# Optimization experiments

Measured on AMD Instinct MI355X. Metric: run time of the kernel, lower is better.

The kernel has to match this reference:

```python
import jax, jax.numpy as jnp
import numpy as np

B, S, D, H = 2, 2048, 1024, 16
DH = D // H
DFF = 4 * D
EPS = 1e-5


def layernorm(x, g, b):
    mu = jnp.mean(x, axis=-1, keepdims=True)
    var = jnp.mean(jnp.square(x - mu), axis=-1, keepdims=True)
    return (x - mu) * jax.lax.rsqrt(var + EPS) * g + b


def setup_inputs() -> dict:
    key = jax.random.key(0)
    ks = jax.random.split(key, 12)
    s = 0.02
    return {
        "x": jax.random.normal(ks[0], (B, S, D), dtype=jnp.float32),
        "ln1_g": jnp.ones((D,), jnp.float32),
        "ln1_b": jnp.zeros((D,), jnp.float32),
        "Wq": jax.random.normal(ks[1], (D, D), jnp.float32) * s,
        "bq": jnp.zeros((D,), jnp.float32),
        "Wk": jax.random.normal(ks[2], (D, D), jnp.float32) * s,
        "bk": jnp.zeros((D,), jnp.float32),
        "Wv": jax.random.normal(ks[3], (D, D), jnp.float32) * s,
        "bv": jnp.zeros((D,), jnp.float32),
        "Wo": jax.random.normal(ks[4], (D, D), jnp.float32) * s,
        "bo": jnp.zeros((D,), jnp.float32),
        "ln2_g": jnp.ones((D,), jnp.float32),
        "ln2_b": jnp.zeros((D,), jnp.float32),
        "W1": jax.random.normal(ks[5], (D, DFF), jnp.float32) * s,
        "b1": jnp.zeros((DFF,), jnp.float32),
        "W2": jax.random.normal(ks[6], (DFF, D), jnp.float32) * s,
        "b2": jnp.zeros((D,), jnp.float32),
    }


def block(x, ln1_g, ln1_b, Wq, bq, Wk, bk, Wv, bv, Wo, bo, ln2_g, ln2_b, W1, b1, W2, b2):
    h = layernorm(x, ln1_g, ln1_b)
    # projections -> [B, H, S, DH]
    q = (h @ Wq + bq).reshape(B, S, H, DH).transpose(0, 2, 1, 3)
    k = (h @ Wk + bk).reshape(B, S, H, DH).transpose(0, 2, 1, 3)
    v = (h @ Wv + bv).reshape(B, S, H, DH).transpose(0, 2, 1, 3)
    scores = jnp.einsum('bhqd,bhkd->bhqk', q, k) / jnp.sqrt(jnp.float32(DH))
    causal = jnp.tril(jnp.ones((S, S), dtype=bool))  # True = keep
    scores = jnp.where(causal, scores, -jnp.inf)
    attn = jax.nn.softmax(scores, axis=-1)
    out = jnp.einsum('bhqk,bhkd->bhqd', attn, v)
    out = out.transpose(0, 2, 1, 3).reshape(B, S, D)
    x = x + out @ Wo + bo
    h2 = layernorm(x, ln2_g, ln2_b)
    ff = jax.nn.gelu(h2 @ W1 + b1, approximate=False) @ W2 + b2
    return x + ff


def reference(x, ln1_g, ln1_b, Wq, bq, Wk, bk, Wv, bv, Wo, bo, ln2_g, ln2_b, W1, b1, W2, b2):
    return block(x, ln1_g, ln1_b, Wq, bq, Wk, bk, Wv, bv, Wo, bo, ln2_g, ln2_b, W1, b1, W2, b2)
```

## Files before the change

kernel.cpp:

```cpp
#include <hip/hip_runtime.h>
#include <cstdint>
#include <cstddef>


#define DEV static __device__ __forceinline__

typedef unsigned short u16;
typedef __bf16 bf16x8 __attribute__((ext_vector_type(8)));
typedef u16    u16x8  __attribute__((ext_vector_type(8)));
typedef u16    u16x4  __attribute__((ext_vector_type(4)));
typedef float  f32x4  __attribute__((ext_vector_type(4)));

#define AEXP2(x) __builtin_amdgcn_exp2f(x)

DEV u16 f2bfh(float f) {
  return __builtin_bit_cast(u16, (__bf16)f);
}

DEV void gl16(const void* g, void* l) {
  __builtin_amdgcn_global_load_lds(
      (const __attribute__((address_space(1))) unsigned*)g,
      (__attribute__((address_space(3))) unsigned*)l, 16, 0, 0);
}

__global__ __launch_bounds__(256)
void tconv(const float* __restrict__ in, u16* __restrict__ out, int R, int C)
{
  __shared__ float tile[32][33];
  const int tx = threadIdx.x & 31, ty = threadIdx.x >> 5;
  const int r0 = blockIdx.y * 32, c0 = blockIdx.x * 32;
#pragma unroll
  for (int i = 0; i < 4; ++i)
    tile[ty + 8*i][tx] = in[(size_t)(r0 + ty + 8*i) * C + c0 + tx];
  __syncthreads();
#pragma unroll
  for (int i = 0; i < 4; ++i)
    out[(size_t)(c0 + ty + 8*i) * R + r0 + tx] = f2bfh(tile[tx][ty + 8*i]);
}

__global__ __launch_bounds__(256)
void tconv4(const float* __restrict__ w0, const float* __restrict__ w1,
            const float* __restrict__ w2, const float* __restrict__ w3,
            u16* __restrict__ q0, u16* __restrict__ q1,
            u16* __restrict__ q2, u16* __restrict__ q3)
{
  __shared__ float tile[32][33];
  const int z = blockIdx.z;
  const float* in = z == 0 ? w0 : z == 1 ? w1 : z == 2 ? w2 : w3;
  u16* out       = z == 0 ? q0 : z == 1 ? q1 : z == 2 ? q2 : q3;
  const int tx = threadIdx.x & 31, ty = threadIdx.x >> 5;
  const int r0 = blockIdx.y * 32, c0 = blockIdx.x * 32;
#pragma unroll
  for (int i = 0; i < 4; ++i)
    tile[ty + 8*i][tx] = in[(size_t)(r0 + ty + 8*i) * 1024 + c0 + tx];
  __syncthreads();
#pragma unroll
  for (int i = 0; i < 4; ++i)
    out[(size_t)(c0 + ty + 8*i) * 1024 + r0 + tx] = f2bfh(tile[tx][ty + 8*i]);
}

__global__ __launch_bounds__(256)
void ln_fwd(const float* __restrict__ x, const float* __restrict__ g,
            const float* __restrict__ b, u16* __restrict__ out)
{
  const int row = blockIdx.x, t = threadIdx.x;
  const float4 v = ((const float4*)(x + (size_t)row * 1024))[t];
  float s1 = v.x + v.y + v.z + v.w;
  float s2 = v.x*v.x + v.y*v.y + v.z*v.z + v.w*v.w;
#pragma unroll
  for (int d = 1; d < 64; d <<= 1) {
    s1 += __shfl_xor(s1, d, 64);
    s2 += __shfl_xor(s2, d, 64);
  }
  __shared__ float sh[8];
  const int w = t >> 6;
  if ((t & 63) == 0) { sh[w] = s1; sh[w + 4] = s2; }
  __syncthreads();
  s1 = sh[0] + sh[1] + sh[2] + sh[3];
  s2 = sh[4] + sh[5] + sh[6] + sh[7];
  const float mu  = s1 * (1.0f / 1024.0f);
  const float var = s2 * (1.0f / 1024.0f) - mu * mu;
  const float rs  = rsqrtf(var + 1e-5f);
  const float4 gv = ((const float4*)g)[t];
  const float4 bv = ((const float4*)b)[t];
  u16x4 o;
  o[0] = f2bfh((v.x - mu) * rs * gv.x + bv.x);
  o[1] = f2bfh((v.y - mu) * rs * gv.y + bv.y);
  o[2] = f2bfh((v.z - mu) * rs * gv.z + bv.z);
  o[3] = f2bfh((v.w - mu) * rs * gv.w + bv.w);
  *(u16x4*)(out + (size_t)row * 1024 + t * 4) = o;
}

#define EPI_QKV  0
#define EPI_RES  1
#define EPI_GELU 2

#define QSCALE 0.180421f

template<int EPI>
__global__ __launch_bounds__(512, 2)
void gemm256(const u16* __restrict__ A, const u16* __restrict__ Bt,
             const float* __restrict__ b0, const float* __restrict__ b1,
             const float* __restrict__ b2,
             u16* __restrict__ o0, u16* __restrict__ o1, u16* __restrict__ o2,
             int N, int K)
{
  __shared__ u16 As[3][8192];
  __shared__ u16 Bs[3][8192];
  const int t = threadIdx.x, lane = t & 63, w = t >> 6;
  const int wr = w >> 2, wc = w & 3;
  const int d = blockIdx.x + gridDim.x * blockIdx.y;
  const int rr = d >> 3;
  const int m0 = ((d & 7) * 2 + (rr & 1)) * 256;
  const int n0 = (rr >> 1) * 256;
  const int li = lane & 15, lg = lane >> 4;

  const int srow = t >> 2;
  const int skc  = (t & 3) ^ ((t >> 3) & 3);
  const u16* Ag = A  + (size_t)(m0 + srow) * K + skc * 8;
  const u16* Bg = Bt + (size_t)(n0 + srow) * K + skc * 8;

  auto STG_A = [&](int k0, int b) {
#pragma unroll
    for (int p = 0; p < 2; ++p)
      gl16(Ag + k0 + (size_t)(p * 128) * K, &As[b][t * 8 + p * 4096]);
  };
  auto STG_B = [&](int k0, int b) {
#pragma unroll
    for (int p = 0; p < 2; ++p)
      gl16(Bg + k0 + (size_t)(p * 128) * K, &Bs[b][t * 8 + p * 4096]);
  };

  auto ldsoff = [](int R, int kc) {
    return (R >> 1) * 128 + (R & 1) * 64 + ((kc ^ ((R >> 1) & 3)) << 4);
  };

  f32x4 acc[8][4] = {};
  const int NT = K >> 5;

  STG_A(0, 0);  STG_B(0, 0);
  STG_A(32, 1); STG_B(32, 1);

  int cur = 0, nxt = 2;
  for (int kt = 0; kt < NT; ++kt) {
    if (kt + 1 < NT)
      asm volatile("s_waitcnt vmcnt(4)" ::: "memory");
    else
      asm volatile("s_waitcnt vmcnt(0)" ::: "memory");
    __builtin_amdgcn_s_barrier();
    __builtin_amdgcn_sched_barrier(0);

    const int k2 = (kt + 2) * 32;
    bf16x8 bfr[4], afA[4];
#pragma unroll
    for (int i = 0; i < 4; ++i)
      bfr[i] = *(const bf16x8*)((const char*)Bs[cur] +
                                ldsoff(wc * 64 + i * 16 + li, lg));
#pragma unroll
    for (int i = 0; i < 4; ++i)
      afA[i] = *(const bf16x8*)((const char*)As[cur] +
                                ldsoff(wr * 128 + i * 16 + li, lg));
    if (kt + 2 < NT) STG_A(k2, nxt);
    __builtin_amdgcn_s_setprio(1);
#pragma unroll
    for (int mi = 0; mi < 4; ++mi)
#pragma unroll
      for (int ni = 0; ni < 4; ++ni)
        acc[mi][ni] = __builtin_amdgcn_mfma_f32_16x16x32_bf16(
            afA[mi], bfr[ni], acc[mi][ni], 0, 0, 0);
    __builtin_amdgcn_s_setprio(0);

    bf16x8 afB[4];
#pragma unroll
    for (int i = 0; i < 4; ++i)
      afB[i] = *(const bf16x8*)((const char*)As[cur] +
                                ldsoff(wr * 128 + (4 + i) * 16 + li, lg));
    if (kt + 2 < NT) STG_B(k2, nxt);
    __builtin_amdgcn_s_setprio(1);
#pragma unroll
    for (int mi = 0; mi < 4; ++mi)
#pragma unroll
      for (int ni = 0; ni < 4; ++ni)
        acc[4 + mi][ni] = __builtin_amdgcn_mfma_f32_16x16x32_bf16(
            afB[mi], bfr[ni], acc[4 + mi][ni], 0, 0, 0);
    __builtin_amdgcn_s_setprio(0);

    cur = (cur + 1 == 3) ? 0 : cur + 1;
    nxt = (nxt + 1 == 3) ? 0 : nxt + 1;
  }

  const int crow = wr * 128 + lg * 4;
  const int ccol = wc * 64 + li;

  if (EPI == EPI_QKV) {
    const int which = n0 >> 10;
    const float* bias = which == 0 ? b0 : which == 1 ? b1 : b2;
    const int nn0 = n0 & 1023;
    if (which == 2) {
#pragma unroll
      for (int mi = 0; mi < 8; ++mi)
#pragma unroll
        for (int ni = 0; ni < 4; ++ni) {
          const int gm0 = m0 + crow + mi * 16;
          const int b_ = gm0 >> 11, s_ = gm0 & 2047;
          const int gc = nn0 + ccol + ni * 16;
          const int h_ = gc >> 6, d_ = gc & 63;
          u16x4 pk;
#pragma unroll
          for (int r = 0; r < 4; ++r) pk[r] = f2bfh(acc[mi][ni][r] + bias[gc]);
          *(u16x4*)(o2 + ((size_t)(b_ * 16 + h_) * 64 + d_) * 2048 + s_) = pk;
        }
    } else {
      u16* outp = which == 0 ? o0 : o1;
      const float sc = which == 0 ? QSCALE : 1.0f;
#pragma unroll
      for (int mi = 0; mi < 8; ++mi)
#pragma unroll
        for (int ni = 0; ni < 4; ++ni)
#pragma unroll
          for (int r = 0; r < 4; ++r) {
            const int gm = m0 + crow + mi * 16 + r;
            const int gc = nn0 + ccol + ni * 16;
            const float v = (acc[mi][ni][r] + bias[gc]) * sc;
            const int b_ = gm >> 11, s_ = gm & 2047;
            const int h_ = gc >> 6,  d_ = gc & 63;
            outp[((size_t)(b_ * 16 + h_) * 2048 + s_) * 64 + d_] = f2bfh(v);
          }
    }
  } else {
#pragma unroll
    for (int mi = 0; mi < 8; ++mi)
#pragma unroll
      for (int ni = 0; ni < 4; ++ni)
#pragma unroll
        for (int r = 0; r < 4; ++r) {
          const int gm = m0 + crow + mi * 16 + r;
          const int gn = n0 + ccol + ni * 16;
          const float v = acc[mi][ni][r] + b0[gn];
          const float y = 0.7978845608f * (v + 0.044715f * v * v * v);
          const float e = AEXP2(fminf(y * 2.8853900818f, 80.0f));
          const float gl = v * e * __builtin_amdgcn_rcpf(e + 1.0f);
          o0[(size_t)gm * N + gn] = f2bfh(gl);
        }
  }
}

template<int EPI, int BM, int CM>
__global__ __launch_bounds__(256)
void gemm_bt(const u16* __restrict__ A, const u16* __restrict__ Bt,
             const float* __restrict__ b0, const float* __restrict__ res,
             float* __restrict__ outf, u16* __restrict__ o0,
             int N, int K)
{
  constexpr int MI = BM / 32;
  constexpr int RA = BM / 32;
  static_assert(BM == 64, "vmcnt(6) assumes 6 loads/step");
  __shared__ u16 As[3][BM * 64];
  __shared__ u16 Bs[3][128 * 64];
  const int t = threadIdx.x, lane = t & 63, w = t >> 6;
  const int wr = w >> 1, wc = w & 1;
  const int d = blockIdx.x + gridDim.x * blockIdx.y;
  const int rr = d >> 3;
  const int m0 = ((d & 7) * CM + rr % CM) * BM;
  const int n0 = (rr / CM) * 128;
  const int li = lane & 15, lg = lane >> 4;

  const int srow = t >> 3;
  const int schunk = (t & 7) ^ (srow & 7);
  const u16* Ag = A  + (size_t)(m0 + srow) * K + schunk * 8;
  const u16* Bg = Bt + (size_t)(n0 + srow) * K + schunk * 8;

  auto STG = [&](int k0, int b) {
#pragma unroll
    for (int p = 0; p < RA; ++p)
      gl16(Ag + k0 + (size_t)(p * 32) * K, &As[b][t * 8 + p * 2048]);
#pragma unroll
    for (int p = 0; p < 4; ++p)
      gl16(Bg + k0 + (size_t)(p * 32) * K, &Bs[b][t * 8 + p * 2048]);
  };

  f32x4 acc[MI][4] = {};
  const int swz = (li & 7) << 4;

  auto COMPUTE = [&](int cur) {
#pragma unroll
    for (int ks = 0; ks < 2; ++ks) {
      bf16x8 af[MI], bfr[4];
#pragma unroll
      for (int i = 0; i < MI; ++i) {
        const int Ra = wr * (MI * 16) + i * 16 + li;
        af[i] = *(const bf16x8*)((const char*)As[cur] + Ra * 128 +
                                 ((ks * 64 + lg * 16) ^ swz));
      }
#pragma unroll
      for (int i = 0; i < 4; ++i) {
        const int Rb = wc * 64 + i * 16 + li;
        bfr[i] = *(const bf16x8*)((const char*)Bs[cur] + Rb * 128 +
                                  ((ks * 64 + lg * 16) ^ swz));
      }
#pragma unroll
      for (int mi = 0; mi < MI; ++mi)
#pragma unroll
        for (int ni = 0; ni < 4; ++ni)
          acc[mi][ni] = __builtin_amdgcn_mfma_f32_16x16x32_bf16(
              af[mi], bfr[ni], acc[mi][ni], 0, 0, 0);
    }
  };

  STG(0, 0);
  if (64 < K) STG(64, 1);
  int cur = 0;
  for (int k0 = 0; k0 < K; k0 += 64) {
    if (k0 + 64 < K)
      asm volatile("s_waitcnt vmcnt(6)" ::: "memory");
    else
      asm volatile("s_waitcnt vmcnt(0)" ::: "memory");
    __builtin_amdgcn_s_barrier();
    __builtin_amdgcn_sched_barrier(0);
    COMPUTE(cur);
    if (k0 + 128 < K) {
      int nxt = cur + 2; if (nxt >= 3) nxt -= 3;
      STG(k0 + 128, nxt);
    }
    cur = (cur + 1 == 3) ? 0 : cur + 1;
  }

  const int crow = wr * (MI * 16) + lg * 4;
  const int ccol = wc * 64 + li;
#pragma unroll
  for (int mi = 0; mi < MI; ++mi)
#pragma unroll
    for (int ni = 0; ni < 4; ++ni)
#pragma unroll
      for (int r = 0; r < 4; ++r) {
        const int gm = m0 + crow + mi * 16 + r;
        const int gn = n0 + ccol + ni * 16;
        const float v = acc[mi][ni][r] + b0[gn];
        const size_t o = (size_t)gm * N + gn;
        outf[o] = v + res[o];
      }
}

__global__ __launch_bounds__(512, 4)
void attn_fwd(const u16* __restrict__ qb, const u16* __restrict__ kb,
              const u16* __restrict__ vtb, u16* __restrict__ ob)
{
  __shared__ u16 Ks[2][128 * 64];
  __shared__ u16 Vt[2][64 * 128];
  __shared__ u16 Ps[8][16 * 64];
  const int t = threadIdx.x, w = t >> 6, lane = t & 63;
  const int li = lane & 15, lg = lane >> 4;
  const int bh = blockIdx.y;
  const int bx = blockIdx.x;
  const int qt = (bh & 16) ? (15 - bx) : bx;
  const int q0 = qt * 128;

  const size_t qrow = (size_t)bh * 2048 + q0 + w * 16 + li;
  const bf16x8 aq0 = *(const bf16x8*)(qb + qrow * 64 + lg * 8);
  const bf16x8 aq1 = *(const bf16x8*)(qb + qrow * 64 + lg * 8 + 32);

  f32x4 o[4] = {};
  float mrun[4], lrun[4];
#pragma unroll
  for (int r = 0; r < 4; ++r) { mrun[r] = -1e30f; lrun[r] = 0.0f; }

  const u16* kbase = kb  + (size_t)bh * 2048 * 64;
  const u16* vbase = vtb + (size_t)bh * 64 * 2048;
  const int ntile = qt + 1;

  const int kchunk = (t & 7)  ^ ((t >> 3) & 7);
  const int vchunk = (t & 15) ^ ((t >> 4) & 15);
  const u16* kg = kbase + (size_t)(t >> 3) * 64 + kchunk * 8;
  const u16* vg = vbase + (size_t)(t >> 4) * 2048 + vchunk * 8;

#define STAGE(tk_, b_)                                              \
  {                                                                 \
    const int kv0s = (tk_) * 128;                                   \
    gl16(kg + (size_t)kv0s * 64,        &Ks[b_][t * 8]);            \
    gl16(kg + (size_t)(kv0s + 64) * 64, &Ks[b_][t * 8 + 4096]);     \
    gl16(vg + kv0s,                     &Vt[b_][t * 8]);            \
    gl16(vg + kv0s + (size_t)32 * 2048, &Vt[b_][t * 8 + 4096]);     \
  }

  STAGE(0, 0);
  __syncthreads();

  for (int tk = 0; tk < ntile; ++tk) {
    const int cur = tk & 1;
    const int kv0 = tk * 128;
    if (tk + 1 < ntile) STAGE(tk + 1, 1 - cur);

    f32x4 s[8];
    __builtin_amdgcn_s_setprio(1);
#pragma unroll
    for (int cf = 0; cf < 8; ++cf) {
      const int row = cf * 16 + li;
      const char* kc = (const char*)Ks[cur] + row * 128;
      const int sw = (row & 7) << 4;
      const bf16x8 bk0 = *(const bf16x8*)(kc + ((lg * 16)      ^ sw));
      const bf16x8 bk1 = *(const bf16x8*)(kc + ((lg * 16 + 64) ^ sw));
      f32x4 z = {};
      z = __builtin_amdgcn_mfma_f32_16x16x32_bf16(aq0, bk0, z, 0, 0, 0);
      z = __builtin_amdgcn_mfma_f32_16x16x32_bf16(aq1, bk1, z, 0, 0, 0);
      s[cf] = z;
    }
    __builtin_amdgcn_s_setprio(0);
    const int row0 = q0 + w * 16 + lg * 4;
    if (tk == ntile - 1) {
#pragma unroll
      for (int cf = 0; cf < 8; ++cf)
#pragma unroll
        for (int r = 0; r < 4; ++r)
          if (kv0 + cf * 16 + li > row0 + r) s[cf][r] = -1e30f;
    }

    float pmax[4];
#pragma unroll
    for (int r = 0; r < 4; ++r) {
      const float a = fmaxf(fmaxf(s[0][r], s[1][r]), fmaxf(s[2][r], s[3][r]));
      const float b = fmaxf(fmaxf(s[4][r], s[5][r]), fmaxf(s[6][r], s[7][r]));
      pmax[r] = fmaxf(a, b);
    }
    bool need = false;
#pragma unroll
    for (int r = 0; r < 4; ++r) need = need || (pmax[r] > mrun[r] + 11.5f);
    if (__any((int)need)) {
#pragma unroll
      for (int d = 1; d < 16; d <<= 1)
#pragma unroll
        for (int r = 0; r < 4; ++r)
          pmax[r] = fmaxf(pmax[r], __shfl_xor(pmax[r], d, 64));
#pragma unroll
      for (int r = 0; r < 4; ++r) {
        const float mnew = fmaxf(mrun[r], pmax[r]);
        const float scl  = AEXP2(mrun[r] - mnew);
        lrun[r] *= scl;
#pragma unroll
        for (int n = 0; n < 4; ++n) o[n][r] *= scl;
        mrun[r] = mnew;
      }
    }
#pragma unroll
    for (int cf = 0; cf < 8; ++cf)
#pragma unroll
      for (int r = 0; r < 4; ++r) {
        const float pv = AEXP2(s[cf][r] - mrun[r]);
        s[cf][r] = pv;
        lrun[r] += pv;
      }

#pragma unroll
    for (int kh = 0; kh < 2; ++kh) {
#pragma unroll
      for (int cf2 = 0; cf2 < 4; ++cf2)
#pragma unroll
        for (int r = 0; r < 4; ++r) {
          const int prow = lg * 4 + r;
          const int pcolB = (cf2 * 16 + li) * 2;
          *(u16*)((char*)Ps[w] + prow * 128 + (pcolB ^ ((prow & 7) << 4))) =
              f2bfh(s[kh * 4 + cf2][r]);
        }
      __builtin_amdgcn_s_setprio(1);
#pragma unroll
      for (int ks = 0; ks < 2; ++ks) {
        const char* pc = (const char*)Ps[w] + li * 128;
        const bf16x8 ap =
            *(const bf16x8*)(pc + ((lg * 16 + ks * 64) ^ ((li & 7) << 4)));
#pragma unroll
        for (int n = 0; n < 4; ++n) {
          const int vrow = n * 16 + li;
          const char* vc = (const char*)Vt[cur] + vrow * 256;
          const int colB = lg * 16 + ks * 64 + kh * 128;
          const bf16x8 bv =
              *(const bf16x8*)(vc + (colB ^ ((vrow & 15) << 4)));
          o[n] = __builtin_amdgcn_mfma_f32_16x16x32_bf16(ap, bv, o[n], 0, 0, 0);
        }
      }
      __builtin_amdgcn_s_setprio(0);
    }

    __syncthreads();
  }
#undef STAGE

#pragma unroll
  for (int d = 1; d < 16; d <<= 1)
#pragma unroll
    for (int r = 0; r < 4; ++r)
      lrun[r] += __shfl_xor(lrun[r], d, 64);

  float inv[4];
#pragma unroll
  for (int r = 0; r < 4; ++r) inv[r] = __builtin_amdgcn_rcpf(lrun[r]);
  const int b_ = bh >> 4, h_ = bh & 15;
#pragma unroll
  for (int n = 0; n < 4; ++n)
#pragma unroll
    for (int r = 0; r < 4; ++r) {
      const int rowg = q0 + w * 16 + lg * 4 + r;
      ob[((size_t)b_ * 2048 + rowg) * 1024 + h_ * 64 + n * 16 + li] =
          f2bfh(o[n][r] * inv[r]);
    }
}

extern "C" void kernel_launch(void* const* d_in, const int* in_sizes, int n_in,
                              void* d_out, int out_size, void* d_ws, size_t ws_size,
                              hipStream_t stream) {
  const float* x    = (const float*)d_in[0];
  const float* ln1g = (const float*)d_in[1];
  const float* ln1b = (const float*)d_in[2];
  const float* Wq   = (const float*)d_in[3];
  const float* bq   = (const float*)d_in[4];
  const float* Wk   = (const float*)d_in[5];
  const float* bk   = (const float*)d_in[6];
  const float* Wv   = (const float*)d_in[7];
  const float* bv   = (const float*)d_in[8];
  const float* Wo   = (const float*)d_in[9];
  const float* bo   = (const float*)d_in[10];
  const float* ln2g = (const float*)d_in[11];
  const float* ln2b = (const float*)d_in[12];
  const float* W1   = (const float*)d_in[13];
  const float* b1   = (const float*)d_in[14];
  const float* W2   = (const float*)d_in[15];
  const float* b2   = (const float*)d_in[16];

  char* ws = (char*)d_ws;
  const size_t MB = 1u << 20;
  u16*   hb   = (u16*)(ws + 0);
  u16*   Wqt  = (u16*)(ws + 8  * MB);
  u16*   Wkt  = (u16*)(ws + 10 * MB);
  u16*   Wvt  = (u16*)(ws + 12 * MB);
  u16*   Wot  = (u16*)(ws + 14 * MB);
  u16*   W1t  = (u16*)(ws + 16 * MB);
  u16*   W2t  = (u16*)(ws + 24 * MB);
  u16*   qbuf = (u16*)(ws + 32 * MB);
  u16*   kbuf = (u16*)(ws + 40 * MB);
  u16*   aob  = (u16*)(ws + 48 * MB);
  u16*   vtb  = (u16*)(ws + 56 * MB);
  float* x2   = (float*)(ws + 64 * MB);
  u16*   h2   = hb;
  u16*   ff1  = qbuf;

  const dim3 blk(256);
  tconv4<<<dim3(32, 32, 4), blk, 0, stream>>>(Wq, Wk, Wv, Wo, Wqt, Wkt, Wvt, Wot);
  tconv<<<dim3(128, 32), blk, 0, stream>>>(W1, W1t, 1024, 4096);
  tconv<<<dim3(32, 128), blk, 0, stream>>>(W2, W2t, 4096, 1024);

  ln_fwd<<<4096, blk, 0, stream>>>(x, ln1g, ln1b, hb);

  gemm256<EPI_QKV><<<dim3(12, 16), dim3(512), 0, stream>>>(
      hb, Wqt, bq, bk, bv, qbuf, kbuf, vtb, 3072, 1024);

  attn_fwd<<<dim3(16, 32), dim3(512), 0, stream>>>(qbuf, kbuf, vtb, aob);

  gemm_bt<EPI_RES, 64, 8><<<dim3(8, 64), blk, 0, stream>>>(
      aob, Wot, bo, x, x2, nullptr, 1024, 1024);

  ln_fwd<<<4096, blk, 0, stream>>>(x2, ln2g, ln2b, h2);

  gemm256<EPI_GELU><<<dim3(16, 16), dim3(512), 0, stream>>>(
      h2, W1t, b1, nullptr, nullptr, ff1, nullptr, nullptr, 4096, 1024);

  gemm_bt<EPI_RES, 64, 8><<<dim3(8, 64), blk, 0, stream>>>(
      ff1, W2t, b2, x2, (float*)d_out, nullptr, 1024, 4096);
}
```

Measured before the change: 207.4 us.

## Replace 64x128 residual GEMM with 128x128 tile using interleaved staging

The output-projection and FFN-down GEMMs move from a 64x128 tile with a 64-wide K step to a 128x128 tile with a 32-wide K step. Each iteration is split into two MFMA halves, and the A and B prefetch loads are interleaved between them under s_setprio. This mirrors the gemm256 pipeline. The larger tile raises operand reuse per block, but the grid drops from 512 to 256 blocks, which may leave the 256 CUs less well filled.

```diff
diff --git a/kernel.cpp b/kernel.cpp
--- a/kernel.cpp
+++ b/kernel.cpp
@@ -97,6 +97,10 @@
 
 #define QSCALE 0.180421f
 
+DEV int ldsoff(int R, int kc) {
+  return (R >> 1) * 128 + (R & 1) * 64 + ((kc ^ ((R >> 1) & 3)) << 4);
+}
+
 template<int EPI>
 __global__ __launch_bounds__(512, 2)
 void gemm256(const u16* __restrict__ A, const u16* __restrict__ Bt,
@@ -131,10 +135,6 @@
       gl16(Bg + k0 + (size_t)(p * 128) * K, &Bs[b][t * 8 + p * 4096]);
   };
 
-  auto ldsoff = [](int R, int kc) {
-    return (R >> 1) * 128 + (R & 1) * 64 + ((kc ^ ((R >> 1) & 3)) << 4);
-  };
-
   f32x4 acc[8][4] = {};
   const int NT = K >> 5;
 
@@ -245,90 +245,94 @@
   }
 }
 
-template<int EPI, int BM, int CM>
 __global__ __launch_bounds__(256)
-void gemm_bt(const u16* __restrict__ A, const u16* __restrict__ Bt,
+void gemm128(const u16* __restrict__ A, const u16* __restrict__ Bt,
              const float* __restrict__ b0, const float* __restrict__ res,
-             float* __restrict__ outf, u16* __restrict__ o0,
-             int N, int K)
+             float* __restrict__ outf, int N, int K)
 {
-  constexpr int MI = BM / 32;
-  constexpr int RA = BM / 32;
-  static_assert(BM == 64, "vmcnt(6) assumes 6 loads/step");
-  __shared__ u16 As[3][BM * 64];
-  __shared__ u16 Bs[3][128 * 64];
+  __shared__ u16 As[3][4096];
+  __shared__ u16 Bs[3][4096];
   const int t = threadIdx.x, lane = t & 63, w = t >> 6;
   const int wr = w >> 1, wc = w & 1;
-  const int d = blockIdx.x + gridDim.x * blockIdx.y;
-  const int rr = d >> 3;
-  const int m0 = ((d & 7) * CM + rr % CM) * BM;
-  const int n0 = (rr / CM) * 128;
+  const int d = blockIdx.x;
+  const int n0 = (d & 7) * 128;
+  const int m0 = (d >> 3) * 128;
   const int li = lane & 15, lg = lane >> 4;
 
-  const int srow = t >> 3;
-  const int schunk = (t & 7) ^ (srow & 7);
-  const u16* Ag = A  + (size_t)(m0 + srow) * K + schunk * 8;
-  const u16* Bg = Bt + (size_t)(n0 + srow) * K + schunk * 8;
-
-  auto STG = [&](int k0, int b) {
-#pragma unroll
-    for (int p = 0; p < RA; ++p)
-      gl16(Ag + k0 + (size_t)(p * 32) * K, &As[b][t * 8 + p * 2048]);
-#pragma unroll
-    for (int p = 0; p < 4; ++p)
-      gl16(Bg + k0 + (size_t)(p * 32) * K, &Bs[b][t * 8 + p * 2048]);
+  const int srow = t >> 2;
+  const int skc  = (t & 3) ^ ((t >> 3) & 3);
+  const u16* Ag = A  + (size_t)(m0 + srow) * K + skc * 8;
+  const u16* Bg = Bt + (size_t)(n0 + srow) * K + skc * 8;
+
+  auto STG_A = [&](int k0, int b) {
+#pragma unroll
+    for (int p = 0; p < 2; ++p)
+      gl16(Ag + k0 + (size_t)(p * 64) * K, &As[b][t * 8 + p * 2048]);
   };
-
-  f32x4 acc[MI][4] = {};
-  const int swz = (li & 7) << 4;
-
-  auto COMPUTE = [&](int cur) {
-#pragma unroll
-    for (int ks = 0; ks < 2; ++ks) {
-      bf16x8 af[MI], bfr[4];
-#pragma unroll
-      for (int i = 0; i < MI; ++i) {
-        const int Ra = wr * (MI * 16) + i * 16 + li;
-        af[i] = *(const bf16x8*)((const char*)As[cur] + Ra * 128 +
-                                 ((ks * 64 + lg * 16) ^ swz));
-      }
-#pragma unroll
-      for (int i = 0; i < 4; ++i) {
-        const int Rb = wc * 64 + i * 16 + li;
-        bfr[i] = *(const bf16x8*)((const char*)Bs[cur] + Rb * 128 +
-                                  ((ks * 64 + lg * 16) ^ swz));
-      }
-#pragma unroll
-      for (int mi = 0; mi < MI; ++mi)
-#pragma unroll
-        for (int ni = 0; ni < 4; ++ni)
-          acc[mi][ni] = __builtin_amdgcn_mfma_f32_16x16x32_bf16(
-              af[mi], bfr[ni], acc[mi][ni], 0, 0, 0);
-    }
+  auto STG_B = [&](int k0, int b) {
+#pragma unroll
+    for (int p = 0; p < 2; ++p)
+      gl16(Bg + k0 + (size_t)(p * 64) * K, &Bs[b][t * 8 + p * 2048]);
   };
 
-  STG(0, 0);
-  if (64 < K) STG(64, 1);
-  int cur = 0;
-  for (int k0 = 0; k0 < K; k0 += 64) {
-    if (k0 + 64 < K)
-      asm volatile("s_waitcnt vmcnt(6)" ::: "memory");
+  f32x4 acc[4][4] = {};
+  const int NT = K >> 5;
+
+  STG_A(0, 0);  STG_B(0, 0);
+  STG_A(32, 1); STG_B(32, 1);
+
+  int cur = 0, nxt = 2;
+  for (int kt = 0; kt < NT; ++kt) {
+    if (kt + 1 < NT)
+      asm volatile("s_waitcnt vmcnt(4)" ::: "memory");
     else
       asm volatile("s_waitcnt vmcnt(0)" ::: "memory");
     __builtin_amdgcn_s_barrier();
     __builtin_amdgcn_sched_barrier(0);
-    COMPUTE(cur);
-    if (k0 + 128 < K) {
-      int nxt = cur + 2; if (nxt >= 3) nxt -= 3;
-      STG(k0 + 128, nxt);
-    }
+
+    const int k2 = (kt + 2) * 32;
+    bf16x8 bfr[4], afA[2];
+#pragma unroll
+    for (int i = 0; i < 4; ++i)
+      bfr[i] = *(const bf16x8*)((const char*)Bs[cur] +
+                                ldsoff(wc * 64 + i * 16 + li, lg));
+#pragma unroll
+    for (int i = 0; i < 2; ++i)
+      afA[i] = *(const bf16x8*)((const char*)As[cur] +
+                                ldsoff(wr * 64 + i * 16 + li, lg));
+    if (kt + 2 < NT) STG_A(k2, nxt);
+    __builtin_amdgcn_s_setprio(1);
+#pragma unroll
+    for (int mi = 0; mi < 2; ++mi)
+#pragma unroll
+      for (int ni = 0; ni < 4; ++ni)
+        acc[mi][ni] = __builtin_amdgcn_mfma_f32_16x16x32_bf16(
+            afA[mi], bfr[ni], acc[mi][ni], 0, 0, 0);
+    __builtin_amdgcn_s_setprio(0);
+
+    bf16x8 afB[2];
+#pragma unroll
+    for (int i = 0; i < 2; ++i)
+      afB[i] = *(const bf16x8*)((const char*)As[cur] +
+                                ldsoff(wr * 64 + (2 + i) * 16 + li, lg));
+    if (kt + 2 < NT) STG_B(k2, nxt);
+    __builtin_amdgcn_s_setprio(1);
+#pragma unroll
+    for (int mi = 0; mi < 2; ++mi)
+#pragma unroll
+      for (int ni = 0; ni < 4; ++ni)
+        acc[2 + mi][ni] = __builtin_amdgcn_mfma_f32_16x16x32_bf16(
+            afB[mi], bfr[ni], acc[2 + mi][ni], 0, 0, 0);
+    __builtin_amdgcn_s_setprio(0);
+
     cur = (cur + 1 == 3) ? 0 : cur + 1;
+    nxt = (nxt + 1 == 3) ? 0 : nxt + 1;
   }
 
-  const int crow = wr * (MI * 16) + lg * 4;
+  const int crow = wr * 64 + lg * 4;
   const int ccol = wc * 64 + li;
 #pragma unroll
-  for (int mi = 0; mi < MI; ++mi)
+  for (int mi = 0; mi < 4; ++mi)
 #pragma unroll
     for (int ni = 0; ni < 4; ++ni)
 #pragma unroll
@@ -553,14 +557,12 @@
 
   attn_fwd<<<dim3(16, 32), dim3(512), 0, stream>>>(qbuf, kbuf, vtb, aob);
 
-  gemm_bt<EPI_RES, 64, 8><<<dim3(8, 64), blk, 0, stream>>>(
-      aob, Wot, bo, x, x2, nullptr, 1024, 1024);
+  gemm128<<<dim3(256), blk, 0, stream>>>(aob, Wot, bo, x, x2, 1024, 1024);
 
   ln_fwd<<<4096, blk, 0, stream>>>(x2, ln2g, ln2b, h2);
 
   gemm256<EPI_GELU><<<dim3(16, 16), dim3(512), 0, stream>>>(
       h2, W1t, b1, nullptr, nullptr, ff1, nullptr, nullptr, 4096, 1024);
 
-  gemm_bt<EPI_RES, 64, 8><<<dim3(8, 64), blk, 0, stream>>>(
-      ff1, W2t, b2, x2, (float*)d_out, nullptr, 1024, 4096);
-}
+  gemm128<<<dim3(256), blk, 0, stream>>>(ff1, W2t, b2, x2, (float*)d_out, 1024, 4096);
+}
```

Result: slower. 255.4 us (+23.1%).
